# Performance work log

Hardware: AMD Instinct MI355X
Metric: run time of the kernel (lower is better)

## Reference

```python
import jax, jax.numpy as jnp
from jax import lax
import numpy as np

NEG = -1e9  # masked_fill value in the torch module


def _cell(x, h, c, Wih, Whh, bih, bhh):
    # PyTorch LSTM gate order: i, f, g, o
    g = x @ Wih.T + bih + h @ Whh.T + bhh
    i, f, gg, o = jnp.split(g, 4, axis=-1)
    c = jax.nn.sigmoid(f) * c + jax.nn.sigmoid(i) * jnp.tanh(gg)
    h = jax.nn.sigmoid(o) * jnp.tanh(c)
    return h, c


def _lstm_layer(xs, Wih, Whh, bih, bhh, reverse=False):
    # xs: [S, B, in] time-major; returns outputs [S,B,H] and final (h,c)
    B = xs.shape[1]
    H = Whh.shape[1]
    init = (jnp.zeros((B, H), xs.dtype), jnp.zeros((B, H), xs.dtype))
    def step(carry, xt):
        h, c = carry
        h, c = _cell(xt, h, c, Wih, Whh, bih, bhh)
        return (h, c), h
    (h, c), ys = lax.scan(step, init, xs, reverse=reverse)
    return ys, h, c


def setup_inputs() -> dict:
    key = jax.random.key(0)
    ks = jax.random.split(key, 32)
    B, S, T, V, E, H = 128, 256, 256, 512, 256, 512
    def p(k, shape):
        return jax.random.normal(k, shape, jnp.float32) * 0.05
    inp = {}
    inp['source'] = jax.random.randint(ks[0], (B, S), 0, V)
    inp['decoder_inputs'] = jax.random.randint(ks[1], (B, T), 0, V)
    inp['emb'] = p(ks[2], (V, E))
    # encoder layer 0 (input E), stacked [fwd, bwd]
    inp['enc_Wih0'] = p(ks[3], (2, 4 * H, E))
    inp['enc_Whh0'] = p(ks[4], (2, 4 * H, H))
    inp['enc_bih0'] = p(ks[5], (2, 4 * H))
    inp['enc_bhh0'] = p(ks[6], (2, 4 * H))
    # encoder layer 1 (input 2H)
    inp['enc_Wih1'] = p(ks[7], (2, 4 * H, 2 * H))
    inp['enc_Whh1'] = p(ks[8], (2, 4 * H, H))
    inp['enc_bih1'] = p(ks[9], (2, 4 * H))
    inp['enc_bhh1'] = p(ks[10], (2, 4 * H))
    # decoder layer 0 (input E + 2H)
    inp['dec_Wih0'] = p(ks[11], (4 * H, E + 2 * H))
    inp['dec_Whh0'] = p(ks[12], (4 * H, H))
    inp['dec_bih0'] = p(ks[13], (4 * H,))
    inp['dec_bhh0'] = p(ks[14], (4 * H,))
    # decoder layer 1 (input H)
    inp['dec_Wih1'] = p(ks[15], (4 * H, H))
    inp['dec_Whh1'] = p(ks[16], (4 * H, H))
    inp['dec_bih1'] = p(ks[17], (4 * H,))
    inp['dec_bhh1'] = p(ks[18], (4 * H,))
    inp['Wq'] = p(ks[19], (2 * H, H))
    inp['bq'] = p(ks[20], (2 * H,))
    inp['Wout'] = p(ks[21], (V, H))
    inp['bout'] = p(ks[22], (V,))
    return inp


def reference(source, decoder_inputs, emb,
              enc_Wih0, enc_Whh0, enc_bih0, enc_bhh0,
              enc_Wih1, enc_Whh1, enc_bih1, enc_bhh1,
              dec_Wih0, dec_Whh0, dec_bih0, dec_bhh0,
              dec_Wih1, dec_Whh1, dec_bih1, dec_bhh1,
              Wq, bq, Wout, bout):
    emb_z = emb.at[0].set(0.0)  # padding_idx=0 row is zero
    xs = jnp.swapaxes(emb_z[source], 0, 1)  # [S,B,E]
    # ---- bidirectional 2-layer encoder ----
    yf0, hf0, cf0 = _lstm_layer(xs, enc_Wih0[0], enc_Whh0[0], enc_bih0[0], enc_bhh0[0])
    yb0, hb0, cb0 = _lstm_layer(xs, enc_Wih0[1], enc_Whh0[1], enc_bih0[1], enc_bhh0[1], reverse=True)
    y0 = jnp.concatenate([yf0, yb0], axis=-1)  # [S,B,2H]
    yf1, hf1, cf1 = _lstm_layer(y0, enc_Wih1[0], enc_Whh1[0], enc_bih1[0], enc_bhh1[0])
    yb1, hb1, cb1 = _lstm_layer(y0, enc_Wih1[1], enc_Whh1[1], enc_bih1[1], enc_bhh1[1], reverse=True)
    enc_out = jnp.swapaxes(jnp.concatenate([yf1, yb1], axis=-1), 0, 1)  # [B,S,2H]
    # merge bidirectional states by summing over directions (per layer)
    h0, c0 = hf0 + hb0, cf0 + cb0
    h1, c1 = hf1 + hb1, cf1 + cb1
    mask = source != 0  # [B,S]
    toks = decoder_inputs.T  # [T,B]

    def dec_step(carry, tok):
        d0h, d0c, d1h, d1c = carry
        e = emb_z[tok]  # [B,E]
        q = d1h @ Wq.T + bq  # attention query from top-layer hidden, [B,2H]
        scores = jnp.einsum('bsh,bh->bs', enc_out, q)
        scores = jnp.where(mask, scores, NEG)
        attn = jax.nn.softmax(scores, axis=1)
        ctx = jnp.einsum('bs,bsh->bh', attn, enc_out)  # [B,2H]
        x = jnp.concatenate([e, ctx], axis=-1)  # [B,E+2H]
        d0h, d0c = _cell(x, d0h, d0c, dec_Wih0, dec_Whh0, dec_bih0, dec_bhh0)
        d1h, d1c = _cell(d0h, d1h, d1c, dec_Wih1, dec_Whh1, dec_bih1, dec_bhh1)
        logits = d1h @ Wout.T + bout  # [B,V]
        return (d0h, d0c, d1h, d1c), logits

    _, logits = lax.scan(dec_step, (h0, c0, h1, c1), toks)  # [T,B,V]
    return jnp.transpose(logits, (1, 0, 2))  # [B,T,V]
```

## Files before the change

kernel.cpp:

```cpp
#include <hip/hip_runtime.h>

typedef __attribute__((ext_vector_type(4))) float f32x4;
typedef __attribute__((ext_vector_type(8))) short bf16x8;
typedef __attribute__((ext_vector_type(4))) short bf16x4;
typedef __attribute__((ext_vector_type(4))) int i4v;
typedef _Float16 f16;
typedef __attribute__((ext_vector_type(8))) _Float16 f16x8;
typedef __attribute__((ext_vector_type(4))) _Float16 f16x4;

#define DEV static __device__ __forceinline__

constexpr int NB = 128;
constexpr int NS = 256;
constexpr int NT = 256;
constexpr int NV = 512;
constexpr int NH = 512;
constexpr int BH = NB * NH;
constexpr float NEGV = -1e9f;

DEV float bf2f(short u) {
  unsigned int i = ((unsigned int)(unsigned short)u) << 16;
  float f; __builtin_memcpy(&f, &i, 4); return f;
}
DEV short f2bf(float x) {
  unsigned int i; __builtin_memcpy(&i, &x, 4);
  i += 0x7fffu + ((i >> 16) & 1u);
  return (short)(i >> 16);
}
DEV int pk(float x) {
  short h = f2bf(x);
  short l = f2bf(x - bf2f(h));
  return ((int)(unsigned short)h << 16) | (int)(unsigned short)l;
}
DEV float upkf(int v) { return bf2f((short)(v >> 16)) + bf2f((short)(v & 0xffff)); }
DEV float sigm(float x) { return 1.0f / (1.0f + __expf(-x)); }
DEV float tanh_(float x) { return 1.0f - 2.0f / (__expf(2.0f * x) + 1.0f); }
DEV f32x4 mfma16(bf16x8 a, bf16x8 b, f32x4 c) {
  return __builtin_amdgcn_mfma_f32_16x16x32_bf16(a, b, c, 0, 0, 0);
}

DEV int aload_i(const int* p) { return __hip_atomic_load(p, __ATOMIC_RELAXED, __HIP_MEMORY_SCOPE_AGENT); }
DEV void astore_i(int* p, int v) { __hip_atomic_store(p, v, __ATOMIC_RELAXED, __HIP_MEMORY_SCOPE_AGENT); }
DEV unsigned long long aload_l(const unsigned long long* p) {
  return __hip_atomic_load(p, __ATOMIC_RELAXED, __HIP_MEMORY_SCOPE_AGENT);
}
DEV float aload_f(const float* p) { return __hip_atomic_load(p, __ATOMIC_RELAXED, __HIP_MEMORY_SCOPE_AGENT); }
DEV void astore_f(float* p, float v) { __hip_atomic_store(p, v, __ATOMIC_RELAXED, __HIP_MEMORY_SCOPE_AGENT); }

DEV void gbar(int* bars, int sub, int subsz, int nsub, int bc) {
  asm volatile("s_waitcnt vmcnt(0) lgkmcnt(0)" ::: "memory");
  __syncthreads();
  if (threadIdx.x == 0) {
    int a = __hip_atomic_fetch_add(&bars[sub * 16], 1, __ATOMIC_RELAXED, __HIP_MEMORY_SCOPE_AGENT);
    if (a + 1 == subsz * bc)
      __hip_atomic_fetch_add(&bars[128], 1, __ATOMIC_RELAXED, __HIP_MEMORY_SCOPE_AGENT);
    while (aload_i(&bars[128]) < nsub * bc) __builtin_amdgcn_s_sleep(4);
    asm volatile("" ::: "memory");
  }
  __syncthreads();
}

DEV void frag_zero(bf16x8& ah, bf16x8& al) { bf16x8 z{}; ah = z; al = z; }
DEV void frag_f32(const float* p, bf16x8& ah, bf16x8& al) {
  f32x4 a = *(const f32x4*)p, b = *(const f32x4*)(p + 4);
#pragma unroll
  for (int j = 0; j < 4; ++j) {
    short h0 = f2bf(a[j]); ah[j] = h0; al[j] = f2bf(a[j] - bf2f(h0));
    short h1 = f2bf(b[j]); ah[4 + j] = h1; al[4 + j] = f2bf(b[j] - bf2f(h1));
  }
}
DEV void frag_f16(const f16* p, bf16x8& ah, bf16x8& al) {
  f16x8 v = *(const f16x8*)p;
#pragma unroll
  for (int j = 0; j < 8; ++j) {
    float f = (float)v[j];
    short h = f2bf(f); ah[j] = h; al[j] = f2bf(f - bf2f(h));
  }
}
DEV void frag_pka(const int* p, bf16x8& ah, bf16x8& al) {
#pragma unroll
  for (int jj = 0; jj < 4; ++jj) {
    unsigned long long u = aload_l((const unsigned long long*)p + jj);
    int va = (int)u, vb = (int)(u >> 32);
    ah[jj * 2] = (short)(va >> 16); al[jj * 2] = (short)(va & 0xffff);
    ah[jj * 2 + 1] = (short)(vb >> 16); al[jj * 2 + 1] = (short)(vb & 0xffff);
  }
}
DEV void frag_pk(const int* p, bf16x8& ah, bf16x8& al) {
  i4v a = *(const i4v*)p; i4v b = *(const i4v*)(p + 4);
#pragma unroll
  for (int j = 0; j < 4; ++j) {
    ah[j] = (short)(a[j] >> 16); al[j] = (short)(a[j] & 0xffff);
    ah[4 + j] = (short)(b[j] >> 16); al[4 + j] = (short)(b[j] & 0xffff);
  }
}
DEV void frag_ctx4(const float* v00, const float* v01, const float* v10, const float* v11,
                   float a0, float a1, bf16x8& ah, bf16x8& al) {
#pragma unroll
  for (int jj = 0; jj < 4; ++jj) {
    unsigned long long u00 = aload_l((const unsigned long long*)v00 + jj);
    unsigned long long u01 = aload_l((const unsigned long long*)v01 + jj);
    unsigned long long u10 = aload_l((const unsigned long long*)v10 + jj);
    unsigned long long u11 = aload_l((const unsigned long long*)v11 + jj);
    float f0a = __uint_as_float((unsigned)u00) + __uint_as_float((unsigned)u01);
    float f0b = __uint_as_float((unsigned)(u00 >> 32)) + __uint_as_float((unsigned)(u01 >> 32));
    float f1a = __uint_as_float((unsigned)u10) + __uint_as_float((unsigned)u11);
    float f1b = __uint_as_float((unsigned)(u10 >> 32)) + __uint_as_float((unsigned)(u11 >> 32));
    float ma = a0 * f0a + a1 * f1a, mb = a0 * f0b + a1 * f1b;
    short ha = f2bf(ma); ah[jj * 2] = ha; al[jj * 2] = f2bf(ma - bf2f(ha));
    short hb = f2bf(mb); ah[jj * 2 + 1] = hb; al[jj * 2 + 1] = f2bf(mb - bf2f(hb));
  }
}

__global__ void k_init(float* hinit, int* bars) {
  int i = blockIdx.x * 256 + threadIdx.x;
  if (i < 4 * BH) hinit[i] = 0.f;
  if (i < 768) bars[i] = 0;
}
__global__ void k_bias(const float* bi0, const float* bh0, const float* bi1, const float* bh1,
                       const float* dbi0, const float* dbh0, const float* dbi1, const float* dbh1,
                       float* e0, float* e1, float* d0, float* d1) {
  int i = blockIdx.x * 256 + threadIdx.x;
  if (i < 4096) { e0[i] = bi0[i] + bh0[i]; e1[i] = bi1[i] + bh1[i]; }
  if (i < 2048) { d0[i] = dbi0[i] + dbh0[i]; d1[i] = dbi1[i] + dbh1[i]; }
}
__global__ void k_fragW(const float* __restrict__ src, short* __restrict__ dst,
                        int K, long tot) {
  long id = (long)blockIdx.x * 256 + threadIdx.x;
  if (id >= tot) return;
  int l = (int)(id & 63);
  long q = id >> 6;
  int KS = K >> 5;
  int ks = (int)(q % KS);
  long q2 = q / KS;
  int g = (int)(q2 & 3);
  long q3 = q2 >> 2;
  long mat = q3 >> 5;
  int ct = (int)(q3 & 31);
  const float* s = src + (mat * 2048 + g * 512 + ct * 16 + (l & 15)) * (long)K +
                   ks * 32 + (l >> 4) * 8;
  short* d = dst + q * 1024 + l * 8;
#pragma unroll
  for (int j = 0; j < 8; ++j) {
    float x = s[j];
    short h = f2bf(x);
    d[j] = h;
    d[512 + j] = f2bf(x - bf2f(h));
  }
}
__global__ void k_convT(const float* __restrict__ src, int* __restrict__ dst) {
  int i = blockIdx.x * 256 + threadIdx.x;
  int n = i >> 10, k = i & 1023;
  dst[i] = pk(src[k * 512 + n]);
}

template <int LAYER>
__global__ __launch_bounds__(512, 2) void k_enc(
    const int* __restrict__ source, const float* __restrict__ emb,
    const f16* __restrict__ y0in,
    const short* __restrict__ WihP, const short* __restrict__ WhhP,
    const float* __restrict__ bsum,
    int* __restrict__ hbuf, f16* __restrict__ yout,
    float* __restrict__ hinitL, float* __restrict__ pbufE, int* bars) {
  constexpr int EX = LAYER ? 1024 : 256;
  constexpr int XK = EX / 32;
  constexpr int TOT = XK + 16;
  constexpr int HALF = TOT / 2;
  __shared__ short sW[HALF * 1024];
  const int wg = blockIdx.x, tid = threadIdx.x, wv = tid >> 6, lane = tid & 63;
  const int l15 = lane & 15, klane = (lane >> 4) * 8;
  const int xx = wg & 7, ii = wg >> 3;
  const int ct = xx * 4 + (ii & 3), g = (ii >> 2) & 3, dir = (ii >> 4) & 1, kp = (ii >> 5) & 1;
  const int cb = ct * 16;
  const short* wih = WihP + (long)dir * 4096 * EX;
  const short* whh = WhhP + (long)dir * 4096 * 512;
  const float* bs = bsum + dir * 2048;
  for (int i = tid; i < HALF * 128; i += 512) {
    int uu = i >> 7, off = (i & 127) * 8;
    int u = kp * HALF + uu;
    const short* src = (u < XK)
        ? wih + ((long)((ct * 4 + g) * XK + u) << 10) + off
        : whh + ((long)((ct * 4 + g) * 16 + (u - XK)) << 10) + off;
    *(bf16x8*)(sW + uu * 1024 + off) = *(const bf16x8*)src;
  }
  int bc = 0;
  {
    int i = wg * 512 + tid;
    int dp = i >> 16, rr = (i >> 9) & 127, c2 = i & 511;
    astore_i(&hbuf[dp * BH + rr * NH + c2], 0);
  }
  gbar(bars, xx, 64, 8, ++bc);
  const int arow = wv * 16 + l15;
  const int frow = g * 32 + (tid >> 4), fcol = cb + (tid & 15);
  float creg = 0.f;
  for (int t = 0; t < NS; ++t) {
    const int tt = dir ? (NS - 1 - t) : t;
    {
      f32x4 acc = {0.f, 0.f, 0.f, 0.f};
      int tok = 0;
      const float* er = nullptr;
      if (LAYER == 0 && kp == 0) { tok = source[arow * NS + tt]; er = emb + (long)tok * 256; }
      const f16* xr = LAYER ? (y0in + ((long)tt * NB + arow) * 1024 + klane) : nullptr;
      const int* hr = hbuf + (long)(dir * 2 + (t & 1)) * BH + arow * NH + klane;
#pragma unroll
      for (int uu = 0; uu < HALF; ++uu) {
        int u = kp * HALF + uu;
        bf16x8 ah, al;
        if (u < XK) {
          if (LAYER == 0) { if (tok) frag_f32(er + u * 32 + klane, ah, al); else frag_zero(ah, al); }
          else frag_f16(xr + u * 32, ah, al);
        } else {
          frag_pka(hr + (u - XK) * 32, ah, al);
        }
        const short* w = sW + uu * 1024 + lane * 8;
        bf16x8 wh = *(const bf16x8*)w, wl = *(const bf16x8*)(w + 512);
        acc = mfma16(ah, wh, acc);
        acc = mfma16(al, wh, acc);
        acc = mfma16(ah, wl, acc);
      }
#pragma unroll
      for (int r = 0; r < 4; ++r) {
        int row = wv * 16 + ((lane >> 4) << 2) + r;
        astore_f(&pbufE[(((long)(kp * 2 + dir) * 128 + row) << 11) + g * 512 + cb + l15], acc[r]);
      }
    }
    gbar(bars, xx, 64, 8, ++bc);
    if (kp == 0) {
      float g4[4];
#pragma unroll
      for (int gp = 0; gp < 4; ++gp)
        g4[gp] = aload_f(&pbufE[(((long)dir * 128 + frow) << 11) + gp * 512 + fcol]) +
                 aload_f(&pbufE[(((long)(2 + dir) * 128 + frow) << 11) + gp * 512 + fcol]) +
                 bs[gp * 512 + fcol];
      float iv = sigm(g4[0]), fv = sigm(g4[1]), gv = tanh_(g4[2]), ov = sigm(g4[3]);
      float cv = fv * creg + iv * gv; creg = cv;
      float hv = ov * tanh_(cv);
      astore_i(&hbuf[(long)(dir * 2 + ((t + 1) & 1)) * BH + frow * NH + fcol], pk(hv));
      if (LAYER == 0) yout[((long)tt * NB + frow) * 1024 + dir * 512 + fcol] = (f16)hv;
      else           yout[((long)frow * NS + tt) * 1024 + dir * 512 + fcol] = (f16)hv;
      if (t == NS - 1) {
        atomicAdd(&hinitL[frow * NH + fcol], hv);
        atomicAdd(&hinitL[BH + frow * NH + fcol], cv);
      }
    }
    gbar(bars, xx, 64, 8, ++bc);
  }
}

__global__ __launch_bounds__(256) void k_gemm_ap(const f16* __restrict__ A,
    const int* __restrict__ WPk, f16* __restrict__ C) {
  const int mt = blockIdx.x & 511, nt = blockIdx.x >> 9;
  const int wv = threadIdx.x >> 6, lane = threadIdx.x & 63;
  const int l15 = lane & 15, klane = (lane >> 4) * 8;
  const int r0 = mt * 64 + wv * 16, n0 = nt * 64;
  f32x4 acc[4] = {{0,0,0,0},{0,0,0,0},{0,0,0,0},{0,0,0,0}};
  const f16* ar = A + (long)(r0 + l15) * 1024 + klane;
  for (int k = 0; k < 1024; k += 32) {
    bf16x8 ah, al;
    frag_f16(ar + k, ah, al);
#pragma unroll
    for (int g = 0; g < 4; ++g) {
      bf16x8 wh, wl;
      frag_pk(WPk + (long)(n0 + g * 16 + l15) * 1024 + k + klane, wh, wl);
      acc[g] = mfma16(ah, wh, acc[g]);
      acc[g] = mfma16(al, wh, acc[g]);
      acc[g] = mfma16(ah, wl, acc[g]);
    }
  }
#pragma unroll
  for (int g = 0; g < 4; ++g)
#pragma unroll
    for (int r = 0; r < 4; ++r) {
      int m = r0 + ((lane >> 4) << 2) + r;
      C[(long)m * 512 + n0 + g * 16 + l15] = (f16)acc[g][r];
    }
}

__global__ void k_sbias(const f16* __restrict__ eo, const float* __restrict__ bq,
                        float* __restrict__ sb) {
  int row = blockIdx.x * 256 + threadIdx.x;
  const f16* p = eo + (long)row * 1024;
  float acc = 0.f;
  for (int k = 0; k < 1024; k += 8) {
    f16x8 v = *(const f16x8*)(p + k);
#pragma unroll
    for (int j = 0; j < 8; ++j) acc += (float)v[j] * bq[k + j];
  }
  sb[row] = acc;
}

__global__ __launch_bounds__(512, 2) void k_dec(
    const int* __restrict__ dects, const float* __restrict__ emb,
    const int* __restrict__ source,
    const f16* __restrict__ aprime, const float* __restrict__ sbias,
    const f16* __restrict__ eo,
    const short* __restrict__ dW0ih, const short* __restrict__ dW0hh,
    const short* __restrict__ dW1ih, const short* __restrict__ dW1hh,
    const float* __restrict__ db0, const float* __restrict__ db1,
    const float* __restrict__ hinit,
    int* __restrict__ d0h, int* __restrict__ d1h,
    float* __restrict__ attscal, float* __restrict__ attvq,
    f16* __restrict__ d1a, int* bars) {
  __shared__ float s_d1[512];
  __shared__ float s_scp[512];
  __shared__ float s_red[8];
  __shared__ float s_w[128];
  __shared__ f32x4 s_cx[256];
  __shared__ f32x4 sC[4][4][64];
  const int wg = blockIdx.x, tid = threadIdx.x, wv = tid >> 6, lane = tid & 63;
  const int tw = wv & 3, grp = wv >> 2;
  const int l15 = lane & 15, klane = (lane >> 4) * 8;
  int bc = 0;
  if (tid < 256) {
    int idx = wg * 256 + tid;
    astore_i(&d0h[idx], pk(hinit[idx]));
    astore_i(&d1h[idx], pk(hinit[2 * BH + idx]));
  }
  const bool cw = (wg < 64);
  int r0 = 0, cb = 0;
  f32x4 c0 = {0,0,0,0}, c1 = {0,0,0,0};
  if (cw) {
    int xx = wg & 7, ii = wg >> 3;
    cb = (xx * 4 + (ii & 3)) * 16;
    r0 = (ii >> 2) * 64 + tw * 16;
    if (grp == 0) {
#pragma unroll
      for (int r = 0; r < 4; ++r) {
        int row = r0 + ((lane >> 4) << 2) + r;
        c0[r] = hinit[BH + row * NH + cb + l15];
        c1[r] = hinit[3 * BH + row * NH + cb + l15];
      }
    }
  }
  gbar(bars, wg & 7, 32, 8, ++bc);
  const int b = wg >> 1, sh = wg & 1;
  const int arow = r0 + l15, col = cb + l15;
  for (int t = 0; t < NT; ++t) {
    const int cur = t & 1, nxt = cur ^ 1;
    {
      if (tid < 256) {
        unsigned long long u = aload_l((const unsigned long long*)(d1h + cur * BH + b * NH) + tid);
        s_d1[tid * 2] = upkf((int)u);
        s_d1[tid * 2 + 1] = upkf((int)(u >> 32));
      }
      __syncthreads();
      {
        int kq = tid >> 7, sl = tid & 127;
        const f16* ap = aprime + (long)(b * NS + sh * 128 + sl) * 512 + kq * 128;
        const float* sd = s_d1 + kq * 128;
        float acc = 0.f;
#pragma unroll 4
        for (int k = 0; k < 128; k += 8) {
          f16x8 v = *(const f16x8*)(ap + k);
#pragma unroll
          for (int j = 0; j < 8; ++j) acc += (float)v[j] * sd[k + j];
        }
        s_scp[kq * 128 + sl] = acc;
      }
      __syncthreads();
      if (tid < 128) {
        int s = sh * 128 + tid;
        float sv = s_scp[tid] + s_scp[128 + tid] + s_scp[256 + tid] + s_scp[384 + tid];
        sv = (source[b * NS + s] != 0) ? (sv + sbias[b * NS + s]) : NEGV;
        s_scp[tid] = sv;
        float m = sv;
#pragma unroll
        for (int o = 32; o > 0; o >>= 1) m = fmaxf(m, __shfl_xor(m, o, 64));
        if (lane == 0) s_red[wv] = m;
      }
      __syncthreads();
      if (tid < 128) {
        float mc = fmaxf(s_red[0], s_red[1]);
        float pv = __expf(s_scp[tid] - mc);
        s_w[tid] = pv;
#pragma unroll
        for (int o = 32; o > 0; o >>= 1) pv += __shfl_xor(pv, o, 64);
        if (lane == 0) s_red[4 + wv] = pv;
      }
      __syncthreads();
      if (tid == 0) {
        astore_f(&attscal[(b * 2 + sh) * 2 + 0], fmaxf(s_red[0], s_red[1]));
        astore_f(&attscal[(b * 2 + sh) * 2 + 1], s_red[4] + s_red[5]);
      }
      {
        int hs = tid >> 8, dd = (tid & 255) * 4;
        float a0 = 0.f, a1 = 0.f, a2 = 0.f, a3 = 0.f;
        const f16* bp = eo + (long)(b * NS + sh * 128 + hs * 64) * 1024 + dd;
        const float* wp = s_w + hs * 64;
#pragma unroll 8
        for (int sl = 0; sl < 64; ++sl) {
          float w = wp[sl];
          f16x4 v = *(const f16x4*)(bp + (long)sl * 1024);
          a0 += w * (float)v[0]; a1 += w * (float)v[1];
          a2 += w * (float)v[2]; a3 += w * (float)v[3];
        }
        float* op = attvq + (long)(((b * 2 + sh) * 2) + hs) * 1024 + dd;
        astore_f(op + 0, a0); astore_f(op + 1, a1);
        astore_f(op + 2, a2); astore_f(op + 3, a3);
      }
    }
    gbar(bars, wg & 7, 32, 8, ++bc);
    if (cw) {
      float m0 = aload_f(&attscal[(arow * 2 + 0) * 2 + 0]), q0 = aload_f(&attscal[(arow * 2 + 0) * 2 + 1]);
      float m1 = aload_f(&attscal[(arow * 2 + 1) * 2 + 0]), q1 = aload_f(&attscal[(arow * 2 + 1) * 2 + 1]);
      float mm = fmaxf(m0, m1);
      float e0 = __expf(m0 - mm), e1 = __expf(m1 - mm);
      float inv = 1.0f / (e0 * q0 + e1 * q1);
      float al0s = e0 * inv, al1s = e1 * inv;
      const float* av00 = attvq + (long)((arow * 2 + 0) * 2 + 0) * 1024 + klane;
      const float* av01 = av00 + 1024;
      const float* av10 = attvq + (long)((arow * 2 + 1) * 2 + 0) * 1024 + klane;
      const float* av11 = av10 + 1024;
      f32x4 acc[4] = {{0,0,0,0},{0,0,0,0},{0,0,0,0},{0,0,0,0}};
      if (grp == 0) {
        int tok = dects[arow * NT + t];
        const float* er = emb + (long)tok * 256;
#pragma unroll
        for (int ks = 0; ks < 8; ++ks) {
          bf16x8 ah, al;
          if (tok) frag_f32(er + ks * 32 + klane, ah, al); else frag_zero(ah, al);
#pragma unroll
          for (int g = 0; g < 4; ++g) {
            const short* w = dW0ih + ((long)((cb >> 4) * 4 + g) * 40 + ks) * 1024 + lane * 8;
            bf16x8 wh = *(const bf16x8*)w, wl = *(const bf16x8*)(w + 512);
            acc[g] = mfma16(ah, wh, acc[g]);
            acc[g] = mfma16(al, wh, acc[g]);
            acc[g] = mfma16(ah, wl, acc[g]);
          }
        }
#pragma unroll 4
        for (int ks = 0; ks < 20; ++ks) {
          bf16x8 ah, al;
          frag_ctx4(av00 + ks * 32, av01 + ks * 32, av10 + ks * 32, av11 + ks * 32,
                    al0s, al1s, ah, al);
#pragma unroll
          for (int g = 0; g < 4; ++g) {
            const short* w = dW0ih + ((long)((cb >> 4) * 4 + g) * 40 + 8 + ks) * 1024 + lane * 8;
            bf16x8 wh = *(const bf16x8*)w, wl = *(const bf16x8*)(w + 512);
            acc[g] = mfma16(ah, wh, acc[g]);
            acc[g] = mfma16(al, wh, acc[g]);
            acc[g] = mfma16(ah, wl, acc[g]);
          }
        }
      } else {
        const int* h0r = d0h + (long)cur * BH + arow * NH + klane;
#pragma unroll 4
        for (int ks = 20; ks < 32; ++ks) {
          bf16x8 ah, al;
          frag_ctx4(av00 + ks * 32, av01 + ks * 32, av10 + ks * 32, av11 + ks * 32,
                    al0s, al1s, ah, al);
#pragma unroll
          for (int g = 0; g < 4; ++g) {
            const short* w = dW0ih + ((long)((cb >> 4) * 4 + g) * 40 + 8 + ks) * 1024 + lane * 8;
            bf16x8 wh = *(const bf16x8*)w, wl = *(const bf16x8*)(w + 512);
            acc[g] = mfma16(ah, wh, acc[g]);
            acc[g] = mfma16(al, wh, acc[g]);
            acc[g] = mfma16(ah, wl, acc[g]);
          }
        }
#pragma unroll 4
        for (int ks = 0; ks < 16; ++ks) {
          bf16x8 ah, al;
          frag_pka(h0r + ks * 32, ah, al);
#pragma unroll
          for (int g = 0; g < 4; ++g) {
            const short* w = dW0hh + ((long)((cb >> 4) * 4 + g) * 16 + ks) * 1024 + lane * 8;
            bf16x8 wh = *(const bf16x8*)w, wl = *(const bf16x8*)(w + 512);
            acc[g] = mfma16(ah, wh, acc[g]);
            acc[g] = mfma16(al, wh, acc[g]);
            acc[g] = mfma16(ah, wl, acc[g]);
          }
        }
#pragma unroll
        for (int g = 0; g < 4; ++g) sC[tw][g][lane] = acc[g];
      }
      __syncthreads();
      if (grp == 0) {
        int* hw = d0h + (long)nxt * BH;
#pragma unroll
        for (int g = 0; g < 4; ++g) acc[g] += sC[tw][g][lane];
#pragma unroll
        for (int r = 0; r < 4; ++r) {
          int row = r0 + ((lane >> 4) << 2) + r;
          float iv = sigm(acc[0][r] + db0[col]);
          float fv = sigm(acc[1][r] + db0[512 + col]);
          float gv = tanh_(acc[2][r] + db0[1024 + col]);
          float ov = sigm(acc[3][r] + db0[1536 + col]);
          float cv = fv * c0[r] + iv * gv; c0[r] = cv;
          astore_i(&hw[row * NH + col], pk(ov * tanh_(cv)));
        }
      }
    }
    gbar(bars, wg & 7, 32, 8, ++bc);
    if (cw) {
      f32x4 acc[4] = {{0,0,0,0},{0,0,0,0},{0,0,0,0},{0,0,0,0}};
      if (grp == 0) {
        const int* h0n = d0h + (long)nxt * BH + arow * NH + klane;
#pragma unroll 4
        for (int ks = 0; ks < 16; ++ks) {
          bf16x8 ah, al;
          frag_pka(h0n + ks * 32, ah, al);
#pragma unroll
          for (int g = 0; g < 4; ++g) {
            const short* w = dW1ih + ((long)((cb >> 4) * 4 + g) * 16 + ks) * 1024 + lane * 8;
            bf16x8 wh = *(const bf16x8*)w, wl = *(const bf16x8*)(w + 512);
            acc[g] = mfma16(ah, wh, acc[g]);
            acc[g] = mfma16(al, wh, acc[g]);
            acc[g] = mfma16(ah, wl, acc[g]);
          }
        }
      } else {
        const int* h1c = d1h + (long)cur * BH + arow * NH + klane;
#pragma unroll 4
        for (int ks = 0; ks < 16; ++ks) {
          bf16x8 ah, al;
          frag_pka(h1c + ks * 32, ah, al);
#pragma unroll
          for (int g = 0; g < 4; ++g) {
            const short* w = dW1hh + ((long)((cb >> 4) * 4 + g) * 16 + ks) * 1024 + lane * 8;
            bf16x8 wh = *(const bf16x8*)w, wl = *(const bf16x8*)(w + 512);
            acc[g] = mfma16(ah, wh, acc[g]);
            acc[g] = mfma16(al, wh, acc[g]);
            acc[g] = mfma16(ah, wl, acc[g]);
          }
        }
#pragma unroll
        for (int g = 0; g < 4; ++g) sC[tw][g][lane] = acc[g];
      }
      __syncthreads();
      if (grp == 0) {
        int* hw = d1h + (long)nxt * BH;
#pragma unroll
        for (int g = 0; g < 4; ++g) acc[g] += sC[tw][g][lane];
#pragma unroll
        for (int r = 0; r < 4; ++r) {
          int row = r0 + ((lane >> 4) << 2) + r;
          float iv = sigm(acc[0][r] + db1[col]);
          float fv = sigm(acc[1][r] + db1[512 + col]);
          float gv = tanh_(acc[2][r] + db1[1024 + col]);
          float ov = sigm(acc[3][r] + db1[1536 + col]);
          float cv = fv * c1[r] + iv * gv; c1[r] = cv;
          float hv = ov * tanh_(cv);
          astore_i(&hw[row * NH + col], pk(hv));
          d1a[((long)t * NB + row) * 512 + col] = (f16)hv;
        }
      }
    }
    gbar(bars, wg & 7, 32, 8, ++bc);
  }
}

__global__ __launch_bounds__(256) void k_gemm_out(const f16* __restrict__ A,
    const float* __restrict__ Wout, const float* __restrict__ bias, float* __restrict__ out) {
  const int mt = blockIdx.x & 511, nt = blockIdx.x >> 9;
  const int wv = threadIdx.x >> 6, lane = threadIdx.x & 63;
  const int l15 = lane & 15, klane = (lane >> 4) * 8;
  const int r0 = mt * 64 + wv * 16, n0 = nt * 64;
  f32x4 acc[4] = {{0,0,0,0},{0,0,0,0},{0,0,0,0},{0,0,0,0}};
  const f16* ar = A + (long)(r0 + l15) * 512 + klane;
  for (int k = 0; k < 512; k += 32) {
    bf16x8 ah, al;
    frag_f16(ar + k, ah, al);
#pragma unroll
    for (int g = 0; g < 4; ++g) {
      bf16x8 wh, wl;
      frag_f32(Wout + (long)(n0 + g * 16 + l15) * 512 + k + klane, wh, wl);
      acc[g] = mfma16(ah, wh, acc[g]);
      acc[g] = mfma16(al, wh, acc[g]);
      acc[g] = mfma16(ah, wl, acc[g]);
    }
  }
#pragma unroll
  for (int g = 0; g < 4; ++g)
#pragma unroll
    for (int r = 0; r < 4; ++r) {
      int m = r0 + ((lane >> 4) << 2) + r;
      int tt = m >> 7, bb = m & 127;
      int n = n0 + g * 16 + l15;
      out[(long)bb * (NT * NV) + tt * NV + n] = acc[g][r] + bias[n];
    }
}

extern "C" void kernel_launch(void* const* d_in, const int* in_sizes, int n_in,
                              void* d_out, int out_size, void* d_ws, size_t ws_size,
                              hipStream_t stream) {
  char* basep = (char*)d_ws;
  size_t off = 0;
  auto alloc = [&](size_t bytes) -> void* {
    off = (off + 255) & ~(size_t)255;
    void* p = basep + off;
    off += bytes;
    return p;
  };
  int* bars = (int*)alloc(4096);
  float* hinit = (float*)alloc((size_t)4 * BH * 4);
  float* eb0 = (float*)alloc(4096 * 4);
  float* eb1 = (float*)alloc(4096 * 4);
  float* db0 = (float*)alloc(2048 * 4);
  float* db1 = (float*)alloc(2048 * 4);
  int* hbufE = (int*)alloc((size_t)4 * BH * 4);
  float* pbufE = (float*)alloc((size_t)4 * 128 * 2048 * 4);
  char* pA = (char*)alloc((size_t)37748736);
  short* e0ihP = (short*)pA;
  short* e0hhP = (short*)(pA + 4194304);
  short* e1ihP = (short*)(pA + 12582912);
  short* e1hhP = (short*)(pA + 29360128);
  f16* aprime = (f16*)pA;
  char* pB = (char*)alloc((size_t)67108864);
  f16* y0 = (f16*)pB;
  short* d0ihP = (short*)pB;
  short* d0hhP = (short*)(pB + 10485760);
  short* d1ihP = (short*)(pB + 14680064);
  short* d1hhP = (short*)(pB + 18874368);
  int* wqPk = (int*)(pB + 23068672);
  f16* d1a = (f16*)(pB + 25165824);
  int* d0h = (int*)(pB + 58720256);
  int* d1h = (int*)(pB + 59244544);
  float* attvq = (float*)(pB + 59768832);
  float* attscal = (float*)(pB + 61865984);
  float* sbias = (float*)(pB + 61870080);
  if (off > ws_size) return;

  const int* source = (const int*)d_in[0];
  const int* dects = (const int*)d_in[1];
  const float* emb = (const float*)d_in[2];
  f16* eo = (f16*)d_out;

  k_init<<<1024, 256, 0, stream>>>(hinit, bars);
  k_bias<<<16, 256, 0, stream>>>((const float*)d_in[5], (const float*)d_in[6],
                                 (const float*)d_in[9], (const float*)d_in[10],
                                 (const float*)d_in[13], (const float*)d_in[14],
                                 (const float*)d_in[17], (const float*)d_in[18],
                                 eb0, eb1, db0, db1);
  k_fragW<<<512, 256, 0, stream>>>((const float*)d_in[3], e0ihP, 256, 131072);
  k_fragW<<<1024, 256, 0, stream>>>((const float*)d_in[4], e0hhP, 512, 262144);
  k_fragW<<<2048, 256, 0, stream>>>((const float*)d_in[7], e1ihP, 1024, 524288);
  k_fragW<<<1024, 256, 0, stream>>>((const float*)d_in[8], e1hhP, 512, 262144);
  k_enc<0><<<512, 512, 0, stream>>>(source, emb, nullptr, e0ihP, e0hhP, eb0,
                                    hbufE, y0, hinit, pbufE, bars);
  k_enc<1><<<512, 512, 0, stream>>>(nullptr, nullptr, y0, e1ihP, e1hhP, eb1,
                                    hbufE, eo, hinit + 2 * BH, pbufE, bars + 256);
  k_fragW<<<1280, 256, 0, stream>>>((const float*)d_in[11], d0ihP, 1280, 327680);
  k_fragW<<<512, 256, 0, stream>>>((const float*)d_in[12], d0hhP, 512, 131072);
  k_fragW<<<512, 256, 0, stream>>>((const float*)d_in[15], d1ihP, 512, 131072);
  k_fragW<<<512, 256, 0, stream>>>((const float*)d_in[16], d1hhP, 512, 131072);
  k_convT<<<2048, 256, 0, stream>>>((const float*)d_in[19], wqPk);
  k_gemm_ap<<<4096, 256, 0, stream>>>(eo, wqPk, aprime);
  k_sbias<<<128, 256, 0, stream>>>(eo, (const float*)d_in[20], sbias);
  k_dec<<<256, 512, 0, stream>>>(dects, emb, source, aprime, sbias, eo,
                                 d0ihP, d0hhP, d1ihP, d1hhP, db0, db1, hinit,
                                 d0h, d1h, attscal, attvq, d1a, bars + 512);
  k_gemm_out<<<4096, 256, 0, stream>>>(d1a, (const float*)d_in[21],
                                       (const float*)d_in[22], (float*)d_out);
}
```

Baseline: 53.02 ms.

## Split decoder attention across four workgroups per batch row with 512-block grid

The persistent decoder kernel now launches 512 workgroups instead of 256, so each batch row's attention over 256 source positions is split into four 64-position quarters rather than two halves. Each quarter computes its score partials, a local softmax max/sum, and a context partial (halves reduced through shared memory), and the LSTM workers merge four partials instead of two. The intent is to shorten the serial attention phase per timestep by spreading it over more workgroups, which requires 4 blocks per CU via launch bounds. The costs are more threads in each grid barrier, more partial merging, and tighter register limits.

```diff
diff --git a/kernel.cpp b/kernel.cpp
--- a/kernel.cpp
+++ b/kernel.cpp
@@ -94,19 +94,18 @@
     ah[4 + j] = (short)(b[j] >> 16); al[4 + j] = (short)(b[j] & 0xffff);
   }
 }
-DEV void frag_ctx4(const float* v00, const float* v01, const float* v10, const float* v11,
-                   float a0, float a1, bf16x8& ah, bf16x8& al) {
+DEV void frag_ctxq(const float* p0, const float* p1, const float* p2, const float* p3,
+                   float w0, float w1, float w2, float w3, bf16x8& ah, bf16x8& al) {
 #pragma unroll
   for (int jj = 0; jj < 4; ++jj) {
-    unsigned long long u00 = aload_l((const unsigned long long*)v00 + jj);
-    unsigned long long u01 = aload_l((const unsigned long long*)v01 + jj);
-    unsigned long long u10 = aload_l((const unsigned long long*)v10 + jj);
-    unsigned long long u11 = aload_l((const unsigned long long*)v11 + jj);
-    float f0a = __uint_as_float((unsigned)u00) + __uint_as_float((unsigned)u01);
-    float f0b = __uint_as_float((unsigned)(u00 >> 32)) + __uint_as_float((unsigned)(u01 >> 32));
-    float f1a = __uint_as_float((unsigned)u10) + __uint_as_float((unsigned)u11);
-    float f1b = __uint_as_float((unsigned)(u10 >> 32)) + __uint_as_float((unsigned)(u11 >> 32));
-    float ma = a0 * f0a + a1 * f1a, mb = a0 * f0b + a1 * f1b;
+    unsigned long long u0 = aload_l((const unsigned long long*)p0 + jj);
+    unsigned long long u1 = aload_l((const unsigned long long*)p1 + jj);
+    unsigned long long u2 = aload_l((const unsigned long long*)p2 + jj);
+    unsigned long long u3 = aload_l((const unsigned long long*)p3 + jj);
+    float ma = w0 * __uint_as_float((unsigned)u0) + w1 * __uint_as_float((unsigned)u1) +
+               w2 * __uint_as_float((unsigned)u2) + w3 * __uint_as_float((unsigned)u3);
+    float mb = w0 * __uint_as_float((unsigned)(u0 >> 32)) + w1 * __uint_as_float((unsigned)(u1 >> 32)) +
+               w2 * __uint_as_float((unsigned)(u2 >> 32)) + w3 * __uint_as_float((unsigned)(u3 >> 32));
     short ha = f2bf(ma); ah[jj * 2] = ha; al[jj * 2] = f2bf(ma - bf2f(ha));
     short hb = f2bf(mb); ah[jj * 2 + 1] = hb; al[jj * 2 + 1] = f2bf(mb - bf2f(hb));
   }
@@ -289,7 +288,7 @@
   sb[row] = acc;
 }
 
-__global__ __launch_bounds__(512, 2) void k_dec(
+__global__ __launch_bounds__(512, 4) void k_dec(
     const int* __restrict__ dects, const float* __restrict__ emb,
     const int* __restrict__ source,
     const f16* __restrict__ aprime, const float* __restrict__ sbias,
@@ -303,15 +302,14 @@
     f16* __restrict__ d1a, int* bars) {
   __shared__ float s_d1[512];
   __shared__ float s_scp[512];
-  __shared__ float s_red[8];
-  __shared__ float s_w[128];
+  __shared__ float s_w[64];
   __shared__ f32x4 s_cx[256];
   __shared__ f32x4 sC[4][4][64];
   const int wg = blockIdx.x, tid = threadIdx.x, wv = tid >> 6, lane = tid & 63;
   const int tw = wv & 3, grp = wv >> 2;
   const int l15 = lane & 15, klane = (lane >> 4) * 8;
   int bc = 0;
-  if (tid < 256) {
+  if (wg < 256 && tid < 256) {
     int idx = wg * 256 + tid;
     astore_i(&d0h[idx], pk(hinit[idx]));
     astore_i(&d1h[idx], pk(hinit[2 * BH + idx]));
@@ -332,8 +330,8 @@
       }
     }
   }
-  gbar(bars, wg & 7, 32, 8, ++bc);
-  const int b = wg >> 1, sh = wg & 1;
+  gbar(bars, wg & 7, 64, 8, ++bc);
+  const int b = wg >> 2, sq = wg & 3;
   const int arow = r0 + l15, col = cb + l15;
   for (int t = 0; t < NT; ++t) {
     const int cur = t & 1, nxt = cur ^ 1;
@@ -345,72 +343,76 @@
       }
       __syncthreads();
       {
-        int kq = tid >> 7, sl = tid & 127;
-        const f16* ap = aprime + (long)(b * NS + sh * 128 + sl) * 512 + kq * 128;
-        const float* sd = s_d1 + kq * 128;
+        int kq = tid >> 6, sl = tid & 63;
+        const f16* ap = aprime + (long)(b * NS + sq * 64 + sl) * 512 + kq * 64;
+        const float* sd = s_d1 + kq * 64;
         float acc = 0.f;
-#pragma unroll 4
-        for (int k = 0; k < 128; k += 8) {
+#pragma unroll
+        for (int k = 0; k < 64; k += 8) {
           f16x8 v = *(const f16x8*)(ap + k);
 #pragma unroll
           for (int j = 0; j < 8; ++j) acc += (float)v[j] * sd[k + j];
         }
-        s_scp[kq * 128 + sl] = acc;
+        s_scp[kq * 64 + sl] = acc;
       }
       __syncthreads();
-      if (tid < 128) {
-        int s = sh * 128 + tid;
-        float sv = s_scp[tid] + s_scp[128 + tid] + s_scp[256 + tid] + s_scp[384 + tid];
+      if (tid < 64) {
+        int s = sq * 64 + tid;
+        float sv = 0.f;
+#pragma unroll
+        for (int kq = 0; kq < 8; ++kq) sv += s_scp[kq * 64 + tid];
         sv = (source[b * NS + s] != 0) ? (sv + sbias[b * NS + s]) : NEGV;
-        s_scp[tid] = sv;
         float m = sv;
 #pragma unroll
         for (int o = 32; o > 0; o >>= 1) m = fmaxf(m, __shfl_xor(m, o, 64));
-        if (lane == 0) s_red[wv] = m;
+        float p = __expf(sv - m);
+        s_w[tid] = p;
+        float q = p;
+#pragma unroll
+        for (int o = 32; o > 0; o >>= 1) q += __shfl_xor(q, o, 64);
+        if (lane == 0) {
+          astore_f(&attscal[(b * 4 + sq) * 2 + 0], m);
+          astore_f(&attscal[(b * 4 + sq) * 2 + 1], q);
+        }
       }
       __syncthreads();
-      if (tid < 128) {
-        float mc = fmaxf(s_red[0], s_red[1]);
-        float pv = __expf(s_scp[tid] - mc);
-        s_w[tid] = pv;
-#pragma unroll
-        for (int o = 32; o > 0; o >>= 1) pv += __shfl_xor(pv, o, 64);
-        if (lane == 0) s_red[4 + wv] = pv;
-      }
-      __syncthreads();
-      if (tid == 0) {
-        astore_f(&attscal[(b * 2 + sh) * 2 + 0], fmaxf(s_red[0], s_red[1]));
-        astore_f(&attscal[(b * 2 + sh) * 2 + 1], s_red[4] + s_red[5]);
-      }
       {
         int hs = tid >> 8, dd = (tid & 255) * 4;
-        float a0 = 0.f, a1 = 0.f, a2 = 0.f, a3 = 0.f;
-        const f16* bp = eo + (long)(b * NS + sh * 128 + hs * 64) * 1024 + dd;
-        const float* wp = s_w + hs * 64;
+        f32x4 a = {0.f, 0.f, 0.f, 0.f};
+        const f16* bp = eo + (long)(b * NS + sq * 64 + hs * 32) * 1024 + dd;
+        const float* wp = s_w + hs * 32;
 #pragma unroll 8
-        for (int sl = 0; sl < 64; ++sl) {
+        for (int sl = 0; sl < 32; ++sl) {
           float w = wp[sl];
           f16x4 v = *(const f16x4*)(bp + (long)sl * 1024);
-          a0 += w * (float)v[0]; a1 += w * (float)v[1];
-          a2 += w * (float)v[2]; a3 += w * (float)v[3];
-        }
-        float* op = attvq + (long)(((b * 2 + sh) * 2) + hs) * 1024 + dd;
-        astore_f(op + 0, a0); astore_f(op + 1, a1);
-        astore_f(op + 2, a2); astore_f(op + 3, a3);
-      }
-    }
-    gbar(bars, wg & 7, 32, 8, ++bc);
+          a[0] += w * (float)v[0]; a[1] += w * (float)v[1];
+          a[2] += w * (float)v[2]; a[3] += w * (float)v[3];
+        }
+        if (hs) s_cx[tid & 255] = a;
+        __syncthreads();
+        if (!hs) {
+          f32x4 o = s_cx[tid];
+          a[0] += o[0]; a[1] += o[1]; a[2] += o[2]; a[3] += o[3];
+          float* op = attvq + (long)(b * 4 + sq) * 1024 + dd;
+          astore_f(op + 0, a[0]); astore_f(op + 1, a[1]);
+          astore_f(op + 2, a[2]); astore_f(op + 3, a[3]);
+        }
+      }
+    }
+    gbar(bars, wg & 7, 64, 8, ++bc);
     if (cw) {
-      float m0 = aload_f(&attscal[(arow * 2 + 0) * 2 + 0]), q0 = aload_f(&attscal[(arow * 2 + 0) * 2 + 1]);
-      float m1 = aload_f(&attscal[(arow * 2 + 1) * 2 + 0]), q1 = aload_f(&attscal[(arow * 2 + 1) * 2 + 1]);
-      float mm = fmaxf(m0, m1);
-      float e0 = __expf(m0 - mm), e1 = __expf(m1 - mm);
-      float inv = 1.0f / (e0 * q0 + e1 * q1);
-      float al0s = e0 * inv, al1s = e1 * inv;
-      const float* av00 = attvq + (long)((arow * 2 + 0) * 2 + 0) * 1024 + klane;
-      const float* av01 = av00 + 1024;
-      const float* av10 = attvq + (long)((arow * 2 + 1) * 2 + 0) * 1024 + klane;
-      const float* av11 = av10 + 1024;
+      float mq0 = aload_f(&attscal[(arow * 4 + 0) * 2]), qq0 = aload_f(&attscal[(arow * 4 + 0) * 2 + 1]);
+      float mq1 = aload_f(&attscal[(arow * 4 + 1) * 2]), qq1 = aload_f(&attscal[(arow * 4 + 1) * 2 + 1]);
+      float mq2 = aload_f(&attscal[(arow * 4 + 2) * 2]), qq2 = aload_f(&attscal[(arow * 4 + 2) * 2 + 1]);
+      float mq3 = aload_f(&attscal[(arow * 4 + 3) * 2]), qq3 = aload_f(&attscal[(arow * 4 + 3) * 2 + 1]);
+      float mm = fmaxf(fmaxf(mq0, mq1), fmaxf(mq2, mq3));
+      float w0 = __expf(mq0 - mm), w1 = __expf(mq1 - mm), w2 = __expf(mq2 - mm), w3 = __expf(mq3 - mm);
+      float inv = 1.0f / (w0 * qq0 + w1 * qq1 + w2 * qq2 + w3 * qq3);
+      w0 *= inv; w1 *= inv; w2 *= inv; w3 *= inv;
+      const float* av0 = attvq + (long)(arow * 4 + 0) * 1024 + klane;
+      const float* av1 = attvq + (long)(arow * 4 + 1) * 1024 + klane;
+      const float* av2 = attvq + (long)(arow * 4 + 2) * 1024 + klane;
+      const float* av3 = attvq + (long)(arow * 4 + 3) * 1024 + klane;
       f32x4 acc[4] = {{0,0,0,0},{0,0,0,0},{0,0,0,0},{0,0,0,0}};
       if (grp == 0) {
         int tok = dects[arow * NT + t];
@@ -431,8 +433,8 @@
 #pragma unroll 4
         for (int ks = 0; ks < 20; ++ks) {
           bf16x8 ah, al;
-          frag_ctx4(av00 + ks * 32, av01 + ks * 32, av10 + ks * 32, av11 + ks * 32,
-                    al0s, al1s, ah, al);
+          frag_ctxq(av0 + ks * 32, av1 + ks * 32, av2 + ks * 32, av3 + ks * 32,
+                    w0, w1, w2, w3, ah, al);
 #pragma unroll
           for (int g = 0; g < 4; ++g) {
             const short* w = dW0ih + ((long)((cb >> 4) * 4 + g) * 40 + 8 + ks) * 1024 + lane * 8;
@@ -447,8 +449,8 @@
 #pragma unroll 4
         for (int ks = 20; ks < 32; ++ks) {
           bf16x8 ah, al;
-          frag_ctx4(av00 + ks * 32, av01 + ks * 32, av10 + ks * 32, av11 + ks * 32,
-                    al0s, al1s, ah, al);
+          frag_ctxq(av0 + ks * 32, av1 + ks * 32, av2 + ks * 32, av3 + ks * 32,
+                    w0, w1, w2, w3, ah, al);
 #pragma unroll
           for (int g = 0; g < 4; ++g) {
             const short* w = dW0ih + ((long)((cb >> 4) * 4 + g) * 40 + 8 + ks) * 1024 + lane * 8;
@@ -491,7 +493,7 @@
         }
       }
     }
-    gbar(bars, wg & 7, 32, 8, ++bc);
+    gbar(bars, wg & 7, 64, 8, ++bc);
     if (cw) {
       f32x4 acc[4] = {{0,0,0,0},{0,0,0,0},{0,0,0,0},{0,0,0,0}};
       if (grp == 0) {
@@ -546,7 +548,7 @@
         }
       }
     }
-    gbar(bars, wg & 7, 32, 8, ++bc);
+    gbar(bars, wg & 7, 64, 8, ++bc);
   }
 }
 
@@ -647,7 +649,7 @@
   k_convT<<<2048, 256, 0, stream>>>((const float*)d_in[19], wqPk);
   k_gemm_ap<<<4096, 256, 0, stream>>>(eo, wqPk, aprime);
   k_sbias<<<128, 256, 0, stream>>>(eo, (const float*)d_in[20], sbias);
-  k_dec<<<256, 512, 0, stream>>>(dects, emb, source, aprime, sbias, eo,
+  k_dec<<<512, 512, 0, stream>>>(dects, emb, source, aprime, sbias, eo,
                                  d0ihP, d0hhP, d1ihP, d1hhP, db0, db1, hinit,
                                  d0h, d1h, attscal, attvq, d1a, bars + 512);
   k_gemm_out<<<4096, 256, 0, stream>>>(d1a, (const float*)d_in[21],
```

New measurement: 58.15 ms. 1.1x slower.
